# Optimization experiments

Hardware: AMD Instinct MI355X
Metric: run time of the kernel (lower is better)

The kernel has to match this reference:

```python
import jax, jax.numpy as jnp
import numpy as np

TOK_DIM = 512
POS_DIM = 512
N_HEADS = 16
HEAD_DIM = 64
D_MODEL = 1024
INNER = N_HEADS * HEAD_DIM
B, T = 4, 2048


def setup_inputs() -> dict:
    key = jax.random.key(0)
    ks = jax.random.split(key, 5)
    s = 0.02
    return {
        "x": jax.random.normal(ks[0], (B, T, TOK_DIM + POS_DIM), dtype=jnp.float32),
        "Wq": jax.random.normal(ks[1], (POS_DIM, INNER), dtype=jnp.float32) * s,
        "Wk": jax.random.normal(ks[2], (POS_DIM, INNER), dtype=jnp.float32) * s,
        "Wv": jax.random.normal(ks[3], (TOK_DIM, INNER), dtype=jnp.float32) * s,
        "Wo": jax.random.normal(ks[4], (INNER, D_MODEL), dtype=jnp.float32) * s,
    }


def reference(x, Wq, Wk, Wv, Wo):
    b, t, _ = x.shape
    x_tok = x[:, :, :TOK_DIM]
    x_pos = x[:, :, TOK_DIM:]
    # project and split heads: [B, H, T, Dh]
    q = (x_pos @ Wq).reshape(b, t, N_HEADS, HEAD_DIM).transpose(0, 2, 1, 3)
    k = (x_pos @ Wk).reshape(b, t, N_HEADS, HEAD_DIM).transpose(0, 2, 1, 3)
    v = (x_tok @ Wv).reshape(b, t, N_HEADS, HEAD_DIM).transpose(0, 2, 1, 3)
    att = jnp.einsum("bhqd,bhkd->bhqk", q, k) / jnp.sqrt(jnp.float32(HEAD_DIM))
    causal = jnp.tril(jnp.ones((t, t), dtype=bool))
    att = jnp.where(causal, att, -jnp.inf)
    att = jax.nn.softmax(att, axis=-1)
    out = jnp.einsum("bhqk,bhkd->bhqd", att, v)
    out = out.transpose(0, 2, 1, 3).reshape(b, t, INNER)
    return out @ Wo
```

## Files before the change

kernel.cpp:

```cpp
#include <hip/hip_runtime.h>
#include <stdint.h>


typedef unsigned short u16;
typedef __bf16 bf16;
typedef bf16 bf16x8 __attribute__((ext_vector_type(8)));
typedef u16 u16x8 __attribute__((ext_vector_type(8)));
typedef u16 u16x4 __attribute__((ext_vector_type(4)));
typedef float f32x4 __attribute__((ext_vector_type(4)));
typedef uint32_t u32x4 __attribute__((ext_vector_type(4)));

__device__ __forceinline__ u16 cvt_bf16(float f) {
  uint32_t u = __builtin_bit_cast(uint32_t, f);
  u += 0x7FFFu + ((u >> 16) & 1u);
  return (u16)(u >> 16);
}

__device__ __forceinline__ uint32_t pack2_bf16(float lo, float hi) {
  uint32_t a = __builtin_bit_cast(uint32_t, lo) + 0x8000u;
  uint32_t b = __builtin_bit_cast(uint32_t, hi) + 0x8000u;
  return __builtin_amdgcn_perm(b, a, 0x07060302u);
}

__device__ __forceinline__ f32x4 mfma_bf(bf16x8 a, bf16x8 b, f32x4 c) {
  return __builtin_amdgcn_mfma_f32_16x16x32_bf16(a, b, c, 0, 0, 0);
}

typedef __attribute__((address_space(1))) const uint32_t g_u32;
typedef __attribute__((address_space(3))) uint32_t l_u32;
__device__ __forceinline__ void gload16(const u16* g, u16* l) {
  __builtin_amdgcn_global_load_lds((g_u32*)g, (l_u32*)l, 16, 0, 0);
}

__global__ __launch_bounds__(256) void prep_x(
    const float* __restrict__ x, u16* __restrict__ xtok,
    u16* __restrict__ xpos) {
  int idx = blockIdx.x * 256 + threadIdx.x;
  int row = idx >> 8;
  int c4 = (idx & 255) * 4;
  float4 v = *(const float4*)(x + (size_t)row * 1024 + c4);
  u16x4 b = {cvt_bf16(v.x), cvt_bf16(v.y), cvt_bf16(v.z), cvt_bf16(v.w)};
  u16* dst = (c4 < 512) ? (xtok + (size_t)row * 512 + c4)
                        : (xpos + (size_t)row * 512 + c4 - 512);
  *(u16x4*)dst = b;
}

__global__ __launch_bounds__(256) void prep_w(
    const float* __restrict__ Wq, const float* __restrict__ Wk,
    const float* __restrict__ Wv, const float* __restrict__ Wo,
    u16* __restrict__ Wt, u16* __restrict__ WoT) {
  const int z = blockIdx.z;
  const float* src = (z == 0) ? Wq : (z == 1) ? Wk : (z == 2) ? Wv : Wo;
  const int K = (z == 3) ? 1024 : 512;
  u16* dst = (z == 3) ? WoT : (Wt + (size_t)z * 1024 * 512);
  const int k0 = blockIdx.y * 64, n0 = blockIdx.x * 64;
  if (k0 >= K) return;
  __shared__ u16 T[64][68];
  const int tid = threadIdx.x;
  const int r = tid >> 4, c = (tid & 15) * 4;
#pragma unroll
  for (int i = 0; i < 4; i++) {
    float4 v = *(const float4*)(src + (size_t)(k0 + r + i * 16) * 1024 + n0 + c);
    u16x4 b = {cvt_bf16(v.x), cvt_bf16(v.y), cvt_bf16(v.z), cvt_bf16(v.w)};
    *(u16x4*)&T[r + i * 16][c] = b;
  }
  __syncthreads();
#pragma unroll
  for (int i = 0; i < 4; i++) {
    int n = r + i * 16;
    u16x4 v;
#pragma unroll
    for (int j = 0; j < 4; j++) v[j] = T[c + j][n];
    *(u16x4*)(dst + (size_t)(n0 + n) * K + k0 + c) = v;
  }
}


#define MM1(M_, N_, J_) { f32x4 c_ = acc[M_][N_];                            \
  c_ = mfma_bf(af[J_][0], bf[N_][0], c_);                                    \
  c_ = mfma_bf(af[J_][1], bf[N_][1], c_);                                    \
  acc[M_][N_] = c_; }

#define XMM(NB) MM1(0,(NB)+0,0) MM1(0,(NB)+1,0) MM1(1,(NB)+0,1)              \
                MM1(1,(NB)+1,1) MM1(2,(NB)+0,2) MM1(2,(NB)+1,2)              \
                MM1(3,(NB)+0,3) MM1(3,(NB)+1,3)

#define XLDA(P) { const u16* bp_ = rA + (P)*8192;                            \
  af[0][0] = *(const bf16x8*)(bp_ + 0*1024 + colx0);                         \
  af[0][1] = *(const bf16x8*)(bp_ + 0*1024 + colx1);                         \
  af[1][0] = *(const bf16x8*)(bp_ + 1*1024 + colx0);                         \
  af[1][1] = *(const bf16x8*)(bp_ + 1*1024 + colx1);                         \
  af[2][0] = *(const bf16x8*)(bp_ + 2*1024 + colx0);                         \
  af[2][1] = *(const bf16x8*)(bp_ + 2*1024 + colx1);                         \
  af[3][0] = *(const bf16x8*)(bp_ + 3*1024 + colx0);                         \
  af[3][1] = *(const bf16x8*)(bp_ + 3*1024 + colx1); }

#define XLDB(P, NB) { const u16* bp_ = rB + (P)*16384;                       \
  bf[(NB)+0][0] = *(const bf16x8*)(bp_ + ((NB)+0)*1024 + colx0);             \
  bf[(NB)+0][1] = *(const bf16x8*)(bp_ + ((NB)+0)*1024 + colx1);             \
  bf[(NB)+1][0] = *(const bf16x8*)(bp_ + ((NB)+1)*1024 + colx0);             \
  bf[(NB)+1][1] = *(const bf16x8*)(bp_ + ((NB)+1)*1024 + colx1); }

#define XSTA(P, KT) { const u16* s_ = gA + (KT)*64;                          \
  u16* d_ = lA + (P)*8192;                                                   \
  gload16(s_, d_); gload16(s_ + (size_t)64*Kd, d_ + 4096); }

#define XSTB0(P, KT) { const u16* s_ = gB + (KT)*64;                         \
  u16* d_ = lB + (P)*16384;                                                  \
  gload16(s_, d_); gload16(s_ + (size_t)64*Kd, d_ + 4096); }

#define XSTB1(P, KT) { const u16* s_ = gB + (size_t)128*Kd + (KT)*64;        \
  u16* d_ = lB + (P)*16384 + 8192;                                           \
  gload16(s_, d_); gload16(s_ + (size_t)64*Kd, d_ + 4096); }

#define PH_MID  asm volatile("" ::: "memory"); __builtin_amdgcn_s_barrier(); \
  asm volatile("s_waitcnt lgkmcnt(0)" ::: "memory");                         \
  __builtin_amdgcn_s_setprio(1);

#define PH_END  __builtin_amdgcn_s_setprio(0);                               \
  asm volatile("" ::: "memory"); __builtin_amdgcn_s_barrier();

#define PH_END_VM2  __builtin_amdgcn_s_setprio(0);                           \
  asm volatile("s_waitcnt vmcnt(2)" ::: "memory");                           \
  asm volatile("" ::: "memory"); __builtin_amdgcn_s_barrier();

#define PH_END_VM4  __builtin_amdgcn_s_setprio(0);                           \
  asm volatile("s_waitcnt vmcnt(4)" ::: "memory");                           \
  asm volatile("" ::: "memory"); __builtin_amdgcn_s_barrier();

template <int Kd>
__device__ __forceinline__ void gemm128_core(
    const u16* __restrict__ Aptr, const u16* __restrict__ Bptr,
    int m0, int n0, u16* smem, f32x4 (&acc)[4][4]) {
  constexpr int NKT = Kd / 64;
  constexpr int NI = NKT / 2;
  const int tid = threadIdx.x;
  const int lane = tid & 63;
  const int mrow = lane & 15, quad = lane >> 4;
  const int w = tid >> 6, wm2 = w >> 2, wn4 = w & 3;

  const int lrs = tid >> 3, sp8 = tid & 7;
  const int slog = sp8 ^ (lrs & 7);
  const u16* gA = Aptr + (size_t)(m0 + lrs) * Kd + slog * 8;
  const u16* gB = Bptr + (size_t)(n0 + lrs) * Kd + slog * 8;
  u16* lA = smem + tid * 8;
  u16* lB = smem + 16384 + tid * 8;

  const int colx0 = (quad * 8) ^ ((mrow & 7) * 8);
  const int colx1 = (32 + quad * 8) ^ ((mrow & 7) * 8);
  const u16* rA = smem + (wm2 * 64 + mrow) * 64;
  const u16* rB = smem + 16384 + (wn4 >> 1) * 8192 + ((wn4 & 1) * 64 + mrow) * 64;

  bf16x8 af[4][2], bf[4][2];

  XSTA(0, 0) XSTB0(0, 0) XSTB1(0, 0)
  XSTA(1, 1) XSTB0(1, 1)
  asm volatile("s_waitcnt vmcnt(4)" ::: "memory");
  asm volatile("" ::: "memory");
  __builtin_amdgcn_s_barrier();

  for (int i = 0; i < NI; ++i) {
    const int kt1 = 2 * i + 1;
    const int kt2 = (2 * i + 2 < NKT) ? 2 * i + 2 : NKT - 1;
    const int kt3 = (2 * i + 3 < NKT) ? 2 * i + 3 : NKT - 1;
    XLDA(0) XLDB(0, 0) XSTB1(1, kt1)
    PH_MID XMM(0) PH_END
    XLDB(0, 2) XSTA(0, kt2)
    PH_MID XMM(2) PH_END_VM2
    XLDA(1) XLDB(1, 0) XSTB0(0, kt2)
    PH_MID XMM(0) PH_END
    XLDB(1, 2) XSTB1(0, kt2) XSTA(1, kt3) XSTB0(1, kt3)
    PH_MID XMM(2) PH_END_VM4
  }
  asm volatile("s_waitcnt vmcnt(0)" ::: "memory");
  __builtin_amdgcn_s_barrier();
}

__device__ __forceinline__ void xcd_remap(int& bx, int& by) {
  int flat = blockIdx.x + 4 * blockIdx.y;
  int wg = (flat & 7) * 32 + (flat >> 3);
  bx = wg & 3;
  by = wg >> 2;
}

__global__ __launch_bounds__(512, 1) void gemm_qkv128(
    const u16* __restrict__ xtok, const u16* __restrict__ xpos,
    const u16* __restrict__ Wt, u16* __restrict__ qkv,
    u16* __restrict__ vperm) {
  const int z = blockIdx.z;
  const u16* A = (z == 2) ? xtok : xpos;
  const u16* Bt = Wt + (size_t)z * 1024 * 512;
  u16* outp = qkv + (size_t)z * (64u * 2048u * 64u);
  const float osc = (z == 0) ? 0.18033688011112042f : 1.0f;
  int bx, by;
  xcd_remap(bx, by);
  const int m0 = by * 128, n0 = bx * 256;

  __shared__ __align__(16) u16 smem[49152];
  f32x4 acc[4][4];
#pragma unroll
  for (int i = 0; i < 4; i++)
#pragma unroll
    for (int j = 0; j < 4; j++) acc[i][j] = (f32x4){0.f, 0.f, 0.f, 0.f};

  gemm128_core<512>(A, Bt, m0, n0, smem, acc);

  const int tid = threadIdx.x;
  const int lane = tid & 63;
  const int mrow = lane & 15, quad = lane >> 4;
  const int w = tid >> 6, wm2 = w >> 2, wn4 = w & 3;

  if (z != 2) {
#pragma unroll
    for (int mi = 0; mi < 4; mi++)
#pragma unroll
      for (int ni = 0; ni < 4; ni++)
#pragma unroll
        for (int r = 0; r < 4; r++) {
          int m = m0 + wm2 * 64 + mi * 16 + quad * 4 + r;
          int n = n0 + wn4 * 64 + ni * 16 + mrow;
          int bb = m >> 11, t = m & 2047;
          int h = n >> 6, d = n & 63;
          outp[(((size_t)(bb * 16 + h)) * 2048 + t) * 64 + d] =
              cvt_bf16(acc[mi][ni][r] * osc);
        }
  } else {
#pragma unroll
    for (int mi = 0; mi < 4; mi++)
#pragma unroll
      for (int ni = 0; ni < 4; ni++)
#pragma unroll
        for (int r = 0; r < 4; r++) {
          int m = m0 + wm2 * 64 + mi * 16 + quad * 4 + r;
          int n = n0 + wn4 * 64 + ni * 16 + mrow;
          int bb = m >> 11, t = m & 2047;
          int h = n >> 6, d = n & 63;
          int k6 = t & 63;
          int pos = (k6 & 32) + ((k6 >> 4) & 1) * 4 + ((k6 >> 2) & 3) * 8 +
                    (k6 & 3);
          vperm[(((size_t)(bb * 16 + h)) * 64 + d) * 2048 + (t & ~63) + pos] =
              cvt_bf16(acc[mi][ni][r]);
        }
  }
}

__global__ __launch_bounds__(512, 1) void gemm_out128(
    const u16* __restrict__ Am, const u16* __restrict__ WoT,
    float* __restrict__ out) {
  int bx, by;
  xcd_remap(bx, by);
  const int m0 = by * 128, n0 = bx * 256;

  __shared__ __align__(16) u16 smem[49152];
  f32x4 acc[4][4];
#pragma unroll
  for (int i = 0; i < 4; i++)
#pragma unroll
    for (int j = 0; j < 4; j++) acc[i][j] = (f32x4){0.f, 0.f, 0.f, 0.f};

  gemm128_core<1024>(Am, WoT, m0, n0, smem, acc);

  const int tid = threadIdx.x;
  const int lane = tid & 63;
  const int mrow = lane & 15, quad = lane >> 4;
  const int w = tid >> 6, wm2 = w >> 2, wn4 = w & 3;

#pragma unroll
  for (int mi = 0; mi < 4; mi++)
#pragma unroll
    for (int ni = 0; ni < 4; ni++)
#pragma unroll
      for (int r = 0; r < 4; r++) {
        int m = m0 + wm2 * 64 + mi * 16 + quad * 4 + r;
        int n = n0 + wn4 * 64 + ni * 16 + mrow;
        out[(size_t)m * 1024 + n] = acc[mi][ni][r];
      }
}

__global__ __launch_bounds__(256, 3) void attn(
    const u16* __restrict__ qkv, const u16* __restrict__ vperm,
    u16* __restrict__ aout) {
  const int bh = blockIdx.x;
  const int qt = 15 - blockIdx.y;
  const int bb = bh >> 4, h = bh & 15;
  const u16* Qp = qkv + (size_t)bh * (2048 * 64);
  const u16* Kp = qkv + (size_t)(64 + bh) * (2048 * 64);
  const u16* Vp = vperm + (size_t)bh * (64 * 2048);

  __shared__ __align__(16) u16 smem[2][4][64 * 32];

  const int tid = threadIdx.x;
  const int lane = tid & 63;
  const int w = tid >> 6;
  const int mrow = lane & 15;
  const int quad = lane >> 4;
  const int srow = w * 16 + (lane >> 2);
  const int sc = (lane & 3) * 8;
  const int soff = srow * 32 + sc;

  const u16x8 onesu = {0x3F80, 0x3F80, 0x3F80, 0x3F80,
                       0x3F80, 0x3F80, 0x3F80, 0x3F80};
  const bf16x8 ones = __builtin_bit_cast(bf16x8, onesu);

  const u16* kgb = Kp + (size_t)srow * 64 + sc;
  const u16* vgb = Vp + (size_t)srow * 2048 + sc;

  const int q0 = qt * 128;
  const int nk = 2 * qt + 2;
  const int qw = q0 + w * 32;

  const u16* qbase = Qp + (size_t)(qw + mrow) * 64 + quad * 8;
  const bf16x8 qf00 = *(const bf16x8*)qbase;
  const bf16x8 qf01 = *(const bf16x8*)(qbase + 32);
  const bf16x8 qf10 = *(const bf16x8*)(qbase + 16 * 64);
  const bf16x8 qf11 = *(const bf16x8*)(qbase + 16 * 64 + 32);

  f32x4 o[2][4], ol[2];
#pragma unroll
  for (int g = 0; g < 2; ++g) {
#pragma unroll
    for (int dt = 0; dt < 4; ++dt) o[g][dt] = (f32x4){0.f, 0.f, 0.f, 0.f};
    ol[g] = (f32x4){0.f, 0.f, 0.f, 0.f};
  }

  u16x8 ka0 = *(const u16x8*)kgb;
  u16x8 ka1 = *(const u16x8*)(kgb + 32);
  u16x8 va0 = *(const u16x8*)vgb;
  u16x8 va1 = *(const u16x8*)(vgb + 32);

  for (int it = 0; it < nk; ++it) {
    u16* buf = &smem[it & 1][0][0];
    *(u16x8*)(buf + 0 * 2048 + soff) = ka0;
    *(u16x8*)(buf + 1 * 2048 + soff) = ka1;
    *(u16x8*)(buf + 2 * 2048 + soff) = va0;
    *(u16x8*)(buf + 3 * 2048 + soff) = va1;

    if (it + 1 < nk) {
      const int kn = (it + 1) * 64;
      ka0 = *(const u16x8*)(kgb + (size_t)kn * 64);
      ka1 = *(const u16x8*)(kgb + (size_t)kn * 64 + 32);
      va0 = *(const u16x8*)(vgb + kn);
      va1 = *(const u16x8*)(vgb + kn + 32);
    }

    __syncthreads();

    const int k0 = it * 64;
    if (k0 > qw + 31) continue;

    f32x4 s[2][4];
#pragma unroll
    for (int nt = 0; nt < 4; ++nt) {
      bf16x8 kf0 = *(const bf16x8*)(buf + 0 * 2048 + (nt * 16 + mrow) * 32 + quad * 8);
      bf16x8 kf1 = *(const bf16x8*)(buf + 1 * 2048 + (nt * 16 + mrow) * 32 + quad * 8);
      f32x4 z0 = (f32x4){0.f, 0.f, 0.f, 0.f};
      z0 = mfma_bf(kf0, qf00, z0);
      s[0][nt] = mfma_bf(kf1, qf01, z0);
      f32x4 z1 = (f32x4){0.f, 0.f, 0.f, 0.f};
      z1 = mfma_bf(kf0, qf10, z1);
      s[1][nt] = mfma_bf(kf1, qf11, z1);
    }

    if (k0 + 63 > qw) {
#pragma unroll
      for (int g = 0; g < 2; ++g)
#pragma unroll
        for (int nt = 0; nt < 4; ++nt)
#pragma unroll
          for (int r = 0; r < 4; ++r)
            if (k0 + nt * 16 + quad * 4 + r > qw + g * 16 + mrow)
              s[g][nt][r] = -1e30f;
    }
#pragma unroll
    for (int g = 0; g < 2; ++g)
#pragma unroll
      for (int nt = 0; nt < 4; ++nt)
#pragma unroll
        for (int r = 0; r < 4; ++r)
          s[g][nt][r] = __builtin_amdgcn_exp2f(s[g][nt][r]);

    bf16x8 pf[2][2];
#pragma unroll
    for (int g = 0; g < 2; ++g) {
      u32x4 pw0 = {pack2_bf16(s[g][0][0], s[g][0][1]),
                   pack2_bf16(s[g][0][2], s[g][0][3]),
                   pack2_bf16(s[g][1][0], s[g][1][1]),
                   pack2_bf16(s[g][1][2], s[g][1][3])};
      u32x4 pw1 = {pack2_bf16(s[g][2][0], s[g][2][1]),
                   pack2_bf16(s[g][2][2], s[g][2][3]),
                   pack2_bf16(s[g][3][0], s[g][3][1]),
                   pack2_bf16(s[g][3][2], s[g][3][3])};
      pf[g][0] = __builtin_bit_cast(bf16x8, pw0);
      pf[g][1] = __builtin_bit_cast(bf16x8, pw1);
      ol[g] = mfma_bf(ones, pf[g][0], ol[g]);
      ol[g] = mfma_bf(ones, pf[g][1], ol[g]);
    }

#pragma unroll
    for (int dt = 0; dt < 4; ++dt) {
      bf16x8 vf0 = *(const bf16x8*)(buf + 2 * 2048 + (dt * 16 + mrow) * 32 + quad * 8);
      bf16x8 vf1 = *(const bf16x8*)(buf + 3 * 2048 + (dt * 16 + mrow) * 32 + quad * 8);
      o[0][dt] = mfma_bf(vf0, pf[0][0], o[0][dt]);
      o[0][dt] = mfma_bf(vf1, pf[0][1], o[0][dt]);
      o[1][dt] = mfma_bf(vf0, pf[1][0], o[1][dt]);
      o[1][dt] = mfma_bf(vf1, pf[1][1], o[1][dt]);
    }
  }

  __syncthreads();
  u16* Osh = &smem[0][0][0];

#pragma unroll
  for (int g = 0; g < 2; ++g) {
    const float inv = 1.f / ol[g][0];
#pragma unroll
    for (int dt = 0; dt < 4; ++dt)
#pragma unroll
      for (int r = 0; r < 4; ++r)
        Osh[(w * 32 + g * 16 + mrow) * 72 + dt * 16 + quad * 4 + r] =
            cvt_bf16(o[g][dt][r] * inv);
  }
#pragma unroll
  for (int p = 0; p < 4; ++p) {
    int ql = (lane >> 3) + 8 * p;
    int ch = lane & 7;
    u16x8 v = *(const u16x8*)&Osh[(w * 32 + ql) * 72 + ch * 8];
    int t = q0 + w * 32 + ql;
    *(u16x8*)(aout + ((size_t)(bb * 2048 + t)) * 1024 + h * 64 + ch * 8) = v;
  }
}

extern "C" void kernel_launch(void* const* d_in, const int* in_sizes, int n_in,
                              void* d_out, int out_size, void* d_ws, size_t ws_size,
                              hipStream_t stream) {
  const float* x  = (const float*)d_in[0];
  const float* Wq = (const float*)d_in[1];
  const float* Wk = (const float*)d_in[2];
  const float* Wv = (const float*)d_in[3];
  const float* Wo = (const float*)d_in[4];

  u16* qkv   = (u16*)d_ws;
  u16* vperm = qkv + (size_t)3 * 64 * 2048 * 64;
  u16* aout  = vperm + (size_t)64 * 64 * 2048;
  u16* xtok  = aout + (size_t)8192 * 1024;
  u16* xpos  = xtok + (size_t)8192 * 512;
  u16* Wt    = xpos + (size_t)8192 * 512;
  u16* WoT   = Wt + (size_t)3 * 1024 * 512;
  float* out = (float*)d_out;

  prep_x<<<dim3(8192), dim3(256), 0, stream>>>(x, xtok, xpos);
  prep_w<<<dim3(16, 16, 4), dim3(256), 0, stream>>>(Wq, Wk, Wv, Wo, Wt, WoT);
  gemm_qkv128<<<dim3(4, 64, 3), dim3(512), 0, stream>>>(xtok, xpos, Wt, qkv, vperm);
  attn<<<dim3(64, 16), dim3(256), 0, stream>>>(qkv, vperm, aout);
  gemm_out128<<<dim3(4, 64), dim3(512), 0, stream>>>(aout, WoT, out);
}
```

Baseline: 193.3 us.

## Switch GEMM core to triple-buffered LDS pipeline with one barrier pair per k-tile

Replaces the two-stage, four-phase interleaved GEMM main loop with a three-stage ring buffer in shared memory. Each iteration loads one full k-tile into registers, issues global-to-LDS prefetch two tiles ahead, then runs both MFMA halves between a single pair of barriers. This aims to cut barrier count and give global loads more latency slack. In exchange LDS use rises from 96 KB to 144 KB per block and less load/compute interleaving happens inside each tile.

```diff
diff --git a/kernel.cpp b/kernel.cpp
--- a/kernel.cpp
+++ b/kernel.cpp
@@ -117,15 +117,8 @@
   asm volatile("s_waitcnt lgkmcnt(0)" ::: "memory");                         \
   __builtin_amdgcn_s_setprio(1);
 
-#define PH_END  __builtin_amdgcn_s_setprio(0);                               \
-  asm volatile("" ::: "memory"); __builtin_amdgcn_s_barrier();
-
-#define PH_END_VM2  __builtin_amdgcn_s_setprio(0);                           \
-  asm volatile("s_waitcnt vmcnt(2)" ::: "memory");                           \
-  asm volatile("" ::: "memory"); __builtin_amdgcn_s_barrier();
-
-#define PH_END_VM4  __builtin_amdgcn_s_setprio(0);                           \
-  asm volatile("s_waitcnt vmcnt(4)" ::: "memory");                           \
+#define PH_END_VM6  __builtin_amdgcn_s_setprio(0);                           \
+  asm volatile("s_waitcnt vmcnt(6)" ::: "memory");                           \
   asm volatile("" ::: "memory"); __builtin_amdgcn_s_barrier();
 
 template <int Kd>
@@ -133,44 +126,44 @@
     const u16* __restrict__ Aptr, const u16* __restrict__ Bptr,
     int m0, int n0, u16* smem, f32x4 (&acc)[4][4]) {
   constexpr int NKT = Kd / 64;
-  constexpr int NI = NKT / 2;
   const int tid = threadIdx.x;
   const int lane = tid & 63;
   const int mrow = lane & 15, quad = lane >> 4;
   const int w = tid >> 6, wm2 = w >> 2, wn4 = w & 3;
 
+  u16* As = smem;
+  u16* Bs = smem + 24576;
+
   const int lrs = tid >> 3, sp8 = tid & 7;
   const int slog = sp8 ^ (lrs & 7);
   const u16* gA = Aptr + (size_t)(m0 + lrs) * Kd + slog * 8;
   const u16* gB = Bptr + (size_t)(n0 + lrs) * Kd + slog * 8;
-  u16* lA = smem + tid * 8;
-  u16* lB = smem + 16384 + tid * 8;
+  u16* lA = As + tid * 8;
+  u16* lB = Bs + tid * 8;
 
   const int colx0 = (quad * 8) ^ ((mrow & 7) * 8);
   const int colx1 = (32 + quad * 8) ^ ((mrow & 7) * 8);
-  const u16* rA = smem + (wm2 * 64 + mrow) * 64;
-  const u16* rB = smem + 16384 + (wn4 >> 1) * 8192 + ((wn4 & 1) * 64 + mrow) * 64;
+  const u16* rA = As + (wm2 * 64 + mrow) * 64;
+  const u16* rB = Bs + (wn4 >> 1) * 8192 + ((wn4 & 1) * 64 + mrow) * 64;
 
   bf16x8 af[4][2], bf[4][2];
 
   XSTA(0, 0) XSTB0(0, 0) XSTB1(0, 0)
-  XSTA(1, 1) XSTB0(1, 1)
-  asm volatile("s_waitcnt vmcnt(4)" ::: "memory");
+  XSTA(1, 1) XSTB0(1, 1) XSTB1(1, 1)
+  asm volatile("s_waitcnt vmcnt(6)" ::: "memory");
   asm volatile("" ::: "memory");
   __builtin_amdgcn_s_barrier();
 
-  for (int i = 0; i < NI; ++i) {
-    const int kt1 = 2 * i + 1;
-    const int kt2 = (2 * i + 2 < NKT) ? 2 * i + 2 : NKT - 1;
-    const int kt3 = (2 * i + 3 < NKT) ? 2 * i + 3 : NKT - 1;
-    XLDA(0) XLDB(0, 0) XSTB1(1, kt1)
-    PH_MID XMM(0) PH_END
-    XLDB(0, 2) XSTA(0, kt2)
-    PH_MID XMM(2) PH_END_VM2
-    XLDA(1) XLDB(1, 0) XSTB0(0, kt2)
-    PH_MID XMM(0) PH_END
-    XLDB(1, 2) XSTB1(0, kt2) XSTA(1, kt3) XSTB0(1, kt3)
-    PH_MID XMM(2) PH_END_VM4
+  int p = 0, ps = 2;
+  for (int t = 0; t < NKT; ++t) {
+    const int kt = (t + 2 < NKT) ? t + 2 : NKT - 1;
+    XLDA(p) XLDB(p, 0) XLDB(p, 2)
+    XSTA(ps, kt) XSTB0(ps, kt) XSTB1(ps, kt)
+    PH_MID
+    XMM(0) XMM(2)
+    PH_END_VM6
+    p = (p == 2) ? 0 : p + 1;
+    ps = (ps == 2) ? 0 : ps + 1;
   }
   asm volatile("s_waitcnt vmcnt(0)" ::: "memory");
   __builtin_amdgcn_s_barrier();
@@ -196,7 +189,7 @@
   xcd_remap(bx, by);
   const int m0 = by * 128, n0 = bx * 256;
 
-  __shared__ __align__(16) u16 smem[49152];
+  __shared__ __align__(16) u16 smem[73728];
   f32x4 acc[4][4];
 #pragma unroll
   for (int i = 0; i < 4; i++)
@@ -251,7 +244,7 @@
   xcd_remap(bx, by);
   const int m0 = by * 128, n0 = bx * 256;
 
-  __shared__ __align__(16) u16 smem[49152];
+  __shared__ __align__(16) u16 smem[73728];
   f32x4 acc[4][4];
 #pragma unroll
   for (int i = 0; i < 4; i++)
```

After: 192.0 us. Within noise of the previous version (-0.7%).
